# Optimization experiments

Measured on AMD Instinct MI355X. Metric: run time of the kernel, lower is better.

## Reference

```python
import jax, jax.numpy as jnp
import numpy as np

ALPHA = 0.3  # LeakyReLU negative slope
NEG_INF = -1e9


def setup_inputs() -> dict:
    key = jax.random.key(0)
    k1, k2, k3, k4 = jax.random.split(key, 4)
    B, N, C_IN, C_OUT, H = 4, 2048, 128, 128, 4
    node_feats = jax.random.normal(k1, (B, N, C_IN), dtype=jnp.float32)
    # xavier_uniform with gain 1.414 for projection weight [c_out, c_in]
    limit_w = 1.414 * np.sqrt(6.0 / (C_IN + C_OUT))
    W = jax.random.uniform(k2, (C_OUT, C_IN), minval=-limit_w, maxval=limit_w, dtype=jnp.float32)
    b = jnp.zeros((C_OUT,), dtype=jnp.float32)
    c_head = C_OUT // H
    limit_a = 1.414 * np.sqrt(6.0 / (H + 2 * c_head))
    a = jax.random.uniform(k3, (H, 2 * c_head), minval=-limit_a, maxval=limit_a, dtype=jnp.float32)
    return {"node_feats": node_feats, "W": W, "b": b, "a": a}


def reference(node_feats, W, b, a):
    B, N, _ = node_feats.shape
    H, two_c = a.shape
    c = two_c // 2
    # dynamic adjacency: cosine similarity, sigmoid > 0.5  <=>  sim > 0
    nf = node_feats / jnp.maximum(jnp.linalg.norm(node_feats, axis=-1, keepdims=True), 1e-12)
    sim = jnp.einsum('bid,bjd->bij', nf, nf)            # [B,N,N]
    mask = sim > 0.0                                     # adjacency (sigmoid(sim) > 0.5)
    # projection -> per-head features [B,N,H,c]
    h = (node_feats @ W.T + b).reshape(B, N, H, c)
    # edge score a . [h_i, h_j] decomposes into left/right parts
    a_l, a_r = a[:, :c], a[:, c:]                        # [H,c] each
    s_l = jnp.einsum('bnhc,hc->bnh', h, a_l)             # [B,N,H]
    s_r = jnp.einsum('bnhc,hc->bnh', h, a_r)             # [B,N,H]
    logits = jax.nn.leaky_relu(s_l[:, :, None, :] + s_r[:, None, :, :], ALPHA)  # [B,N,N,H]
    attn = jnp.where(mask[..., None], logits, NEG_INF)
    probs = jax.nn.softmax(attn, axis=2)                 # softmax over source nodes j
    # dropout is identity in eval mode
    out = jnp.einsum('bijh,bjhc->bihc', probs, h)
    return out.reshape(B, N, -1)                         # concat heads
```

## Files before the change

kernel.cpp:

```cpp
#include <hip/hip_runtime.h>
#include <cstdint>
#include <cstddef>

typedef float v16f __attribute__((ext_vector_type(16)));
typedef short v8s  __attribute__((ext_vector_type(8)));

#define MFMA32(A,B,C) __builtin_amdgcn_mfma_f32_32x32x16_bf16((A),(B),(C),0,0,0)
#define THRU 1e-3f

__device__ __forceinline__ unsigned f2bf(float f) {
  unsigned u = __builtin_bit_cast(unsigned, f);
  u += 0x7FFFu + ((u >> 16) & 1u);
  return u >> 16;
}
__device__ __forceinline__ float bf2f(unsigned us) {
  return __builtin_bit_cast(float, us << 16);
}
__device__ __forceinline__ void gload16(const void* g, void* l) {
  __builtin_amdgcn_global_load_lds(
      (const __attribute__((address_space(1))) void*)g,
      (__attribute__((address_space(3))) void*)l, 16, 0, 0);
}

__global__ __launch_bounds__(256) void gat_prep(
    const float* __restrict__ nf, const float* __restrict__ Wm,
    const float* __restrict__ bias, const float* __restrict__ aw,
    unsigned short* __restrict__ nfh, unsigned short* __restrict__ nfm,
    unsigned short* __restrict__ ht,
    float* __restrict__ EFl, float* __restrict__ EFh)
{
  __shared__ float xl[32][132];
  const int tid = threadIdx.x;
  const int row = tid & 31, g = tid >> 5;
  const int r0 = blockIdx.x * 32;
  const int b = r0 >> 11, n0 = r0 & 2047;
  const int d0 = g * 16;

  float x[16];
  {
    const float* xp = nf + (size_t)(r0 + row) * 128 + d0;
#pragma unroll
    for (int q = 0; q < 4; ++q) {
      float4 v = *(const float4*)(xp + 4 * q);
      x[4*q+0] = v.x; x[4*q+1] = v.y; x[4*q+2] = v.z; x[4*q+3] = v.w;
    }
  }
  {
    unsigned hu[16], mu[16];
#pragma unroll
    for (int q = 0; q < 16; ++q) {
      xl[row][d0 + q] = x[q];
      unsigned hb = f2bf(x[q]); float hf = bf2f(hb);
      unsigned mb = f2bf(x[q] - hf);
      hu[q] = hb; mu[q] = mb;
    }
    const size_t to = ((size_t)(b * 64 + (n0 >> 5)) * 8 + g) * 512 + row * 8;
    uint4 p0, p1;
    p0.x = hu[0] | (hu[1] << 16);  p0.y = hu[2] | (hu[3] << 16);
    p0.z = hu[4] | (hu[5] << 16);  p0.w = hu[6] | (hu[7] << 16);
    p1.x = hu[8] | (hu[9] << 16);  p1.y = hu[10] | (hu[11] << 16);
    p1.z = hu[12] | (hu[13] << 16); p1.w = hu[14] | (hu[15] << 16);
    *(uint4*)(nfh + to) = p0; *(uint4*)(nfh + to + 256) = p1;
    p0.x = mu[0] | (mu[1] << 16);  p0.y = mu[2] | (mu[3] << 16);
    p0.z = mu[4] | (mu[5] << 16);  p0.w = mu[6] | (mu[7] << 16);
    p1.x = mu[8] | (mu[9] << 16);  p1.y = mu[10] | (mu[11] << 16);
    p1.z = mu[12] | (mu[13] << 16); p1.w = mu[14] | (mu[15] << 16);
    *(uint4*)(nfm + to) = p0; *(uint4*)(nfm + to + 256) = p1;
  }
  __syncthreads();

  float acc[16];
  const int ob = g * 16;
#pragma unroll
  for (int o = 0; o < 16; ++o) acc[o] = bias[ob + o];
  for (int dd = 0; dd < 128; dd += 4) {
    float4 xq = *(const float4*)&xl[row][dd];
#pragma unroll
    for (int o = 0; o < 16; ++o) {
      float4 wq = *(const float4*)(Wm + (size_t)(ob + o) * 128 + dd);
      acc[o] = fmaf(xq.x, wq.x, acc[o]);
      acc[o] = fmaf(xq.y, wq.y, acc[o]);
      acc[o] = fmaf(xq.z, wq.z, acc[o]);
      acc[o] = fmaf(xq.w, wq.w, acc[o]);
    }
  }
#pragma unroll
  for (int o = 0; o < 16; ++o)
    ht[((size_t)b * 128 + ob + o) * 2048 + n0 + row] = (unsigned short)f2bf(acc[o]);

  const int hh = g >> 1, cb = (g & 1) * 16;
  float sl = 0.f, sr = 0.f;
#pragma unroll
  for (int o = 0; o < 16; ++o) {
    sl = fmaf(acc[o], aw[hh * 64 + cb + o], sl);
    sr = fmaf(acc[o], aw[hh * 64 + 32 + cb + o], sr);
  }
  sl += __shfl_xor(sl, 32, 64);
  sr += __shfl_xor(sr, 32, 64);
  if (!(g & 1)) {
    const float L2E = 1.4426950408889634f;
    float El = exp2f(sl * L2E), Fl = exp2f(sl * (0.3f * L2E));
    float Er = exp2f(sr * L2E), Fr = exp2f(sr * (0.3f * L2E));
    size_t nn = (size_t)(r0 + row);
    EFl[nn * 8 + hh]     = El;
    EFl[nn * 8 + 4 + hh] = Fl;
    const size_t eo = ((size_t)(b * 4 + hh) * 2048 + (n0 + row)) * 2;
    EFh[eo]     = Er;
    EFh[eo + 1] = Fr;
  }
}

__global__ __launch_bounds__(256) void gat_mask(
    const unsigned short* __restrict__ nfh, const unsigned short* __restrict__ nfm,
    const float* __restrict__ nf, unsigned* __restrict__ mask)
{
  const int tid = threadIdx.x, lane = tid & 63;
  const int li = lane & 31, hi = lane >> 5;
  const int blk = blockIdx.x;
  const int jb = blk & 31, t = blk >> 5;
  const int ib = t & 15, b = t >> 4;
  const int i0 = ib * 128 + (tid >> 6) * 32;
  const int j0 = jb * 64;

  const size_t lbyte = (size_t)lane * 8;
  const size_t tiB  = ((size_t)(b * 64 + (i0 >> 5)) * 8) * 512 + lbyte;
  const size_t tjA0 = ((size_t)(b * 64 + (j0 >> 5)) * 8) * 512 + lbyte;
  const size_t tjA1 = tjA0 + 4096;

  v8s BH[8], BM[8];
#pragma unroll
  for (int kc = 0; kc < 8; ++kc) {
    BH[kc] = *(const v8s*)(nfh + tiB + kc * 512);
    BM[kc] = *(const v8s*)(nfm + tiB + kc * 512);
  }

  v16f S0, S1;
#pragma unroll
  for (int r = 0; r < 16; ++r) { S0[r] = 0.f; S1[r] = 0.f; }
#pragma unroll
  for (int kc = 0; kc < 8; ++kc) {
    v8s A0h = *(const v8s*)(nfh + tjA0 + kc * 512);
    v8s A1h = *(const v8s*)(nfh + tjA1 + kc * 512);
    v8s A0m = *(const v8s*)(nfm + tjA0 + kc * 512);
    v8s A1m = *(const v8s*)(nfm + tjA1 + kc * 512);
    S0 = MFMA32(A0h, BH[kc], S0);
    S1 = MFMA32(A1h, BH[kc], S1);
    S0 = MFMA32(A0h, BM[kc], S0);
    S1 = MFMA32(A1h, BM[kc], S1);
    S0 = MFMA32(A0m, BH[kc], S0);
    S1 = MFMA32(A1m, BH[kc], S1);
  }

  unsigned u0 = 0, u1 = 0;
  float mn = 1e30f;
  const int sh = hi * 4;
#pragma unroll
  for (int r = 0; r < 16; ++r) {
    const int jlc = (r & 3) + 8 * (r >> 2);
    const unsigned bit = (1u << jlc) << sh;
    if (S0[r] > 0.f) u0 |= bit;
    if (S1[r] > 0.f) u1 |= bit;
    mn = fminf(mn, fabsf(S0[r]));
    mn = fminf(mn, fabsf(S1[r]));
  }

  if (mn < THRU) {
    const float* xi = nf + ((size_t)b * 2048 + i0 + li) * 128;
#pragma unroll
    for (int sub = 0; sub < 2; ++sub) {
#pragma unroll
      for (int r = 0; r < 16; ++r) {
        const float s = sub ? S1[r] : S0[r];
        if (fabsf(s) < THRU) {
          const int jlc = (r & 3) + 8 * (r >> 2);
          const int j = j0 + sub * 32 + jlc + 4 * hi;
          const float* xj = nf + ((size_t)b * 2048 + j) * 128;
          double a = 0.0;
          for (int k = 0; k < 128; k += 2) {
            a = fma((double)xi[k],     (double)xj[k],     a);
            a = fma((double)xi[k + 1], (double)xj[k + 1], a);
          }
          const unsigned bit = (1u << jlc) << sh;
          if (sub == 0) u0 = (a > 0.0) ? (u0 | bit) : (u0 & ~bit);
          else          u1 = (a > 0.0) ? (u1 | bit) : (u1 & ~bit);
        }
      }
    }
  }

  unsigned f0 = u0 | (unsigned)__shfl_xor((int)u0, 32, 64);
  unsigned f1 = u1 | (unsigned)__shfl_xor((int)u1, 32, 64);
  if (hi == 0) {
    mask[(size_t)(b * 64 + jb * 2)     * 2048 + i0 + li] = f0;
    mask[(size_t)(b * 64 + jb * 2 + 1) * 2048 + i0 + li] = f1;
  }
}

__global__ __launch_bounds__(256, 2) void gat_attn(
    const unsigned short* __restrict__ ht, const float* __restrict__ EFl,
    const float* __restrict__ EFh, const unsigned* __restrict__ mask,
    float* __restrict__ out)
{
  __shared__ __align__(16) char sm[36864];
  const int tid = threadIdx.x, lane = tid & 63, wv = tid >> 6;
  const int li = lane & 31, hi = lane >> 5;

  const int blk = blockIdx.x;
  const int ig = (blk >> 3) & 63;
  const int combo = (blk & 7) * 2 + (blk >> 9);
  const int b = combo >> 2, h = combo & 3;

  const size_t nb = (size_t)b * 2048;
  const int i0 = ig * 32;
  const int j0w = wv * 512;
  char* mybase = sm + wv * 9216;

  const float EL = EFl[(nb + i0 + li) * 8 + h];
  const float FL = EFl[(nb + i0 + li) * 8 + 4 + h];

  unsigned mw[16];
#pragma unroll
  for (int q = 0; q < 16; ++q)
    mw[q] = mask[(size_t)(b * 64 + wv * 16 + q) * 2048 + i0 + li] >> (hi * 4);

  asm volatile("s_waitcnt vmcnt(0)" ::: "memory");
  __builtin_amdgcn_sched_barrier(0);

  const int vrow = lane >> 3, vgs = lane & 7;
  auto STAGE = [&](int h0, int p) {
    const int jbase = j0w + (h0 << 6);
    const size_t srow = (size_t)(b * 128 + h * 32) * 2048 + jbase;
#pragma unroll
    for (int q = 0; q < 4; ++q) {
      const int row = q * 8 + vrow;
      gload16((const char*)(ht + srow + (size_t)row * 2048 + ((vgs ^ (row & 7)) << 3)),
              mybase + p * 4608 + q * 1024);
    }
    if (lane < 32)
      gload16((const char*)EFh + ((size_t)(b * 4 + h) * 2048 + jbase) * 8 + lane * 16,
              mybase + p * 4608 + 4096);
  };

  STAGE(0, 0);

  v16f acc;
#pragma unroll
  for (int r = 0; r < 16; ++r) acc[r] = 0.f;
  float den = 0.f;

#pragma unroll
  for (int h0 = 0; h0 < 8; ++h0) {
    const int p = h0 & 1;
    if (h0 < 7) {
      STAGE(h0 + 1, p ^ 1);
      asm volatile("s_waitcnt vmcnt(5)" ::: "memory");
    } else {
      asm volatile("s_waitcnt vmcnt(0)" ::: "memory");
    }
    __builtin_amdgcn_sched_barrier(0);

    const char* base = mybase + p * 4608;
#pragma unroll
    for (int it2 = 0; it2 < 2; ++it2) {
      const unsigned mh = mw[h0 * 2 + it2];
      const char* Eb = base + 4096 + (it2 << 8);
      unsigned pw[8];
#pragma unroll
      for (int rp = 0; rp < 8; ++rp) {
        const int r0 = 2 * rp;
        const int jl0c = (r0 & 3) + 8 * (r0 >> 2);
        const int off = (jl0c + 4 * hi) * 8;
        float2 e0 = *(const float2*)(Eb + off);
        float2 e1 = *(const float2*)(Eb + off + 8);
        const bool m0 = (mh >> jl0c) & 1;
        const bool m1 = (mh >> (jl0c + 1)) & 1;
        float w0 = fmaxf(e0.x * EL, e0.y * FL); w0 = m0 ? w0 : 0.f;
        float w1 = fmaxf(e1.x * EL, e1.y * FL); w1 = m1 ? w1 : 0.f;
        den += w0 + w1;
        asm("v_cvt_pk_bf16_f32 %0, %1, %2" : "=v"(pw[rp]) : "v"(w0), "v"(w1));
      }
      auto q0 = __builtin_amdgcn_permlane32_swap((int)pw[0], (int)pw[2], false, false);
      auto q1 = __builtin_amdgcn_permlane32_swap((int)pw[1], (int)pw[3], false, false);
      auto q2 = __builtin_amdgcn_permlane32_swap((int)pw[4], (int)pw[6], false, false);
      auto q3 = __builtin_amdgcn_permlane32_swap((int)pw[5], (int)pw[7], false, false);
      uint4 c0, c1;
      c0.x = (unsigned)q0[0]; c0.y = (unsigned)q1[0];
      c0.z = (unsigned)q0[1]; c0.w = (unsigned)q1[1];
      c1.x = (unsigned)q2[0]; c1.y = (unsigned)q3[0];
      c1.z = (unsigned)q2[1]; c1.w = (unsigned)q3[1];
      v8s P0 = __builtin_bit_cast(v8s, c0);
      v8s P1 = __builtin_bit_cast(v8s, c1);
      const char* vr = base + li * 128;
      const int cx = li & 7;
      v8s V0 = *(const v8s*)(vr + ((((it2 << 2) + hi) ^ cx) << 4));
      v8s V1 = *(const v8s*)(vr + ((((it2 << 2) + 2 + hi) ^ cx) << 4));
      acc = MFMA32(P0, V0, acc);
      acc = MFMA32(P1, V1, acc);
    }
  }

  __syncthreads();
  if (wv) {
    float* dst = (float*)sm + (size_t)(wv - 1) * 1088 + lane * 17;
#pragma unroll
    for (int r = 0; r < 16; ++r) dst[r] = acc[r];
    dst[16] = den;
  }
  __syncthreads();
  if (wv == 0) {
#pragma unroll
    for (int w = 0; w < 3; ++w) {
      const float* src = (const float*)sm + (size_t)w * 1088 + lane * 17;
#pragma unroll
      for (int r = 0; r < 16; ++r) acc[r] += src[r];
      den += src[16];
    }
    den += __shfl_xor(den, 32, 64);
    float* dl = (float*)sm + 3 * 1088;
    if (lane < 32) dl[li] = den;
    asm volatile("s_waitcnt lgkmcnt(0)" ::: "memory");
    __builtin_amdgcn_sched_barrier(0);
    const size_t ob = (nb + i0) * 128 + h * 32 + li;
#pragma unroll
    for (int r = 0; r < 16; ++r) {
      const int il = (r & 3) + 8 * (r >> 2) + 4 * hi;
      out[ob + (size_t)il * 128] = acc[r] / dl[il];
    }
  }
}

extern "C" void kernel_launch(void* const* d_in, const int* in_sizes, int n_in,
                              void* d_out, int out_size, void* d_ws, size_t ws_size,
                              hipStream_t stream) {
  const float* nf   = (const float*)d_in[0];
  const float* Wm   = (const float*)d_in[1];
  const float* bias = (const float*)d_in[2];
  const float* aw   = (const float*)d_in[3];
  float* out = (float*)d_out;
  char* ws = (char*)d_ws;

  unsigned short* nfh = (unsigned short*)(ws);
  unsigned short* nfm = (unsigned short*)(ws + 2097152);
  unsigned short* ht  = (unsigned short*)(ws + 4194304);
  float*    EFl  = (float*)(ws + 6291456);
  float*    EFh  = (float*)(ws + 6553600);
  unsigned* mask = (unsigned*)(ws + 6815744);

  gat_prep<<<256, 256, 0, stream>>>(nf, Wm, bias, aw, nfh, nfm, ht, EFl, EFh);
  gat_mask<<<2048, 256, 0, stream>>>(nfh, nfm, nf, mask);
  gat_attn<<<1024, 256, 0, stream>>>(ht, EFl, EFh, mask, out);
}
```

Before: 82.10 us.

## Store projected features in MFMA fragment layout and load directly from global

Result: slower. 88.74 us (+8.1%).

```diff
diff --git a/kernel.cpp b/kernel.cpp
--- a/kernel.cpp
+++ b/kernel.cpp
@@ -16,17 +16,12 @@
 __device__ __forceinline__ float bf2f(unsigned us) {
   return __builtin_bit_cast(float, us << 16);
 }
-__device__ __forceinline__ void gload16(const void* g, void* l) {
-  __builtin_amdgcn_global_load_lds(
-      (const __attribute__((address_space(1))) void*)g,
-      (__attribute__((address_space(3))) void*)l, 16, 0, 0);
-}
 
 __global__ __launch_bounds__(256) void gat_prep(
     const float* __restrict__ nf, const float* __restrict__ Wm,
     const float* __restrict__ bias, const float* __restrict__ aw,
     unsigned short* __restrict__ nfh, unsigned short* __restrict__ nfm,
-    unsigned short* __restrict__ ht,
+    unsigned short* __restrict__ vt,
     float* __restrict__ EFl, float* __restrict__ EFh)
 {
   __shared__ float xl[32][132];
@@ -84,9 +79,16 @@
       acc[o] = fmaf(xq.w, wq.w, acc[o]);
     }
   }
-#pragma unroll
-  for (int o = 0; o < 16; ++o)
-    ht[((size_t)b * 128 + ob + o) * 2048 + n0 + row] = (unsigned short)f2bf(acc[o]);
+  {
+    const int f = (row >> 4) & 1, kh = (row >> 3) & 1, e = row & 7;
+#pragma unroll
+    for (int o = 0; o < 16; ++o) {
+      const int c = ob + o, hh2 = c >> 5, cc = c & 31;
+      const size_t va = (((size_t)(b * 4 + hh2) * 64 + (n0 >> 5)) * 2 + f) * 512
+                        + (kh * 32 + cc) * 8 + e;
+      vt[va] = (unsigned short)f2bf(acc[o]);
+    }
+  }
 
   const int hh = g >> 1, cb = (g & 1) * 16;
   float sl = 0.f, sr = 0.f;
@@ -196,127 +198,100 @@
   }
 }
 
-__global__ __launch_bounds__(256, 2) void gat_attn(
-    const unsigned short* __restrict__ ht, const float* __restrict__ EFl,
+__global__ __launch_bounds__(256) void gat_attn(
+    const unsigned short* __restrict__ vt, const float* __restrict__ EFl,
     const float* __restrict__ EFh, const unsigned* __restrict__ mask,
     float* __restrict__ out)
 {
-  __shared__ __align__(16) char sm[36864];
+  __shared__ __align__(16) float sm[2][64][17];
   const int tid = threadIdx.x, lane = tid & 63, wv = tid >> 6;
   const int li = lane & 31, hi = lane >> 5;
 
   const int blk = blockIdx.x;
-  const int ig = (blk >> 3) & 63;
-  const int combo = (blk & 7) * 2 + (blk >> 9);
+  const int ig = blk & 63;
+  const int combo = blk >> 6;
   const int b = combo >> 2, h = combo & 3;
 
   const size_t nb = (size_t)b * 2048;
   const int i0 = ig * 32;
-  const int j0w = wv * 512;
-  char* mybase = sm + wv * 9216;
 
   const float EL = EFl[(nb + i0 + li) * 8 + h];
   const float FL = EFl[(nb + i0 + li) * 8 + 4 + h];
 
-  unsigned mw[16];
-#pragma unroll
-  for (int q = 0; q < 16; ++q)
-    mw[q] = mask[(size_t)(b * 64 + wv * 16 + q) * 2048 + i0 + li] >> (hi * 4);
-
-  asm volatile("s_waitcnt vmcnt(0)" ::: "memory");
-  __builtin_amdgcn_sched_barrier(0);
-
-  const int vrow = lane >> 3, vgs = lane & 7;
-  auto STAGE = [&](int h0, int p) {
-    const int jbase = j0w + (h0 << 6);
-    const size_t srow = (size_t)(b * 128 + h * 32) * 2048 + jbase;
-#pragma unroll
-    for (int q = 0; q < 4; ++q) {
-      const int row = q * 8 + vrow;
-      gload16((const char*)(ht + srow + (size_t)row * 2048 + ((vgs ^ (row & 7)) << 3)),
-              mybase + p * 4608 + q * 1024);
-    }
-    if (lane < 32)
-      gload16((const char*)EFh + ((size_t)(b * 4 + h) * 2048 + jbase) * 8 + lane * 16,
-              mybase + p * 4608 + 4096);
-  };
-
-  STAGE(0, 0);
+  const unsigned* mrow = mask + (size_t)(b * 64 + wv * 16) * 2048 + i0 + li;
+  const float* efb = EFh + ((size_t)(b * 4 + h) * 2048 + wv * 512) * 2;
+  const unsigned short* vb =
+      vt + ((size_t)(b * 4 + h) * 64 + wv * 16) * 1024 + (size_t)lane * 8;
 
   v16f acc;
 #pragma unroll
   for (int r = 0; r < 16; ++r) acc[r] = 0.f;
-  float den = 0.f;
-
-#pragma unroll
-  for (int h0 = 0; h0 < 8; ++h0) {
-    const int p = h0 & 1;
-    if (h0 < 7) {
-      STAGE(h0 + 1, p ^ 1);
-      asm volatile("s_waitcnt vmcnt(5)" ::: "memory");
-    } else {
-      asm volatile("s_waitcnt vmcnt(0)" ::: "memory");
-    }
-    __builtin_amdgcn_sched_barrier(0);
-
-    const char* base = mybase + p * 4608;
-#pragma unroll
-    for (int it2 = 0; it2 < 2; ++it2) {
-      const unsigned mh = mw[h0 * 2 + it2];
-      const char* Eb = base + 4096 + (it2 << 8);
-      unsigned pw[8];
-#pragma unroll
-      for (int rp = 0; rp < 8; ++rp) {
-        const int r0 = 2 * rp;
-        const int jl0c = (r0 & 3) + 8 * (r0 >> 2);
-        const int off = (jl0c + 4 * hi) * 8;
-        float2 e0 = *(const float2*)(Eb + off);
-        float2 e1 = *(const float2*)(Eb + off + 8);
-        const bool m0 = (mh >> jl0c) & 1;
-        const bool m1 = (mh >> (jl0c + 1)) & 1;
-        float w0 = fmaxf(e0.x * EL, e0.y * FL); w0 = m0 ? w0 : 0.f;
-        float w1 = fmaxf(e1.x * EL, e1.y * FL); w1 = m1 ? w1 : 0.f;
-        den += w0 + w1;
-        asm("v_cvt_pk_bf16_f32 %0, %1, %2" : "=v"(pw[rp]) : "v"(w0), "v"(w1));
-      }
-      auto q0 = __builtin_amdgcn_permlane32_swap((int)pw[0], (int)pw[2], false, false);
-      auto q1 = __builtin_amdgcn_permlane32_swap((int)pw[1], (int)pw[3], false, false);
-      auto q2 = __builtin_amdgcn_permlane32_swap((int)pw[4], (int)pw[6], false, false);
-      auto q3 = __builtin_amdgcn_permlane32_swap((int)pw[5], (int)pw[7], false, false);
-      uint4 c0, c1;
-      c0.x = (unsigned)q0[0]; c0.y = (unsigned)q1[0];
-      c0.z = (unsigned)q0[1]; c0.w = (unsigned)q1[1];
-      c1.x = (unsigned)q2[0]; c1.y = (unsigned)q3[0];
-      c1.z = (unsigned)q2[1]; c1.w = (unsigned)q3[1];
-      v8s P0 = __builtin_bit_cast(v8s, c0);
-      v8s P1 = __builtin_bit_cast(v8s, c1);
-      const char* vr = base + li * 128;
-      const int cx = li & 7;
-      v8s V0 = *(const v8s*)(vr + ((((it2 << 2) + hi) ^ cx) << 4));
-      v8s V1 = *(const v8s*)(vr + ((((it2 << 2) + 2 + hi) ^ cx) << 4));
-      acc = MFMA32(P0, V0, acc);
-      acc = MFMA32(P1, V1, acc);
-    }
-  }
-
-  __syncthreads();
-  if (wv) {
-    float* dst = (float*)sm + (size_t)(wv - 1) * 1088 + lane * 17;
-#pragma unroll
-    for (int r = 0; r < 16; ++r) dst[r] = acc[r];
-    dst[16] = den;
+  float den0 = 0.f, den1 = 0.f;
+
+#pragma unroll 4
+  for (int it2 = 0; it2 < 16; ++it2) {
+    const unsigned mh = mrow[(size_t)it2 * 2048] >> (hi * 4);
+    v8s V0 = *(const v8s*)(vb + it2 * 1024);
+    v8s V1 = *(const v8s*)(vb + it2 * 1024 + 512);
+    unsigned pw[8];
+#pragma unroll
+    for (int rp = 0; rp < 8; ++rp) {
+      const int r0 = 2 * rp;
+      const int jl0c = (r0 & 3) + 8 * (r0 >> 2);
+      const int j2 = it2 * 32 + jl0c + 4 * hi;
+      float4 e01 = *(const float4*)(efb + j2 * 2);
+      const bool m0 = (mh >> jl0c) & 1;
+      const bool m1 = (mh >> (jl0c + 1)) & 1;
+      float w0 = fmaxf(e01.x * EL, e01.y * FL); w0 = m0 ? w0 : 0.f;
+      float w1 = fmaxf(e01.z * EL, e01.w * FL); w1 = m1 ? w1 : 0.f;
+      den0 += w0; den1 += w1;
+      asm("v_cvt_pk_bf16_f32 %0, %1, %2" : "=v"(pw[rp]) : "v"(w0), "v"(w1));
+    }
+    auto q0 = __builtin_amdgcn_permlane32_swap((int)pw[0], (int)pw[2], false, false);
+    auto q1 = __builtin_amdgcn_permlane32_swap((int)pw[1], (int)pw[3], false, false);
+    auto q2 = __builtin_amdgcn_permlane32_swap((int)pw[4], (int)pw[6], false, false);
+    auto q3 = __builtin_amdgcn_permlane32_swap((int)pw[5], (int)pw[7], false, false);
+    uint4 c0, c1;
+    c0.x = (unsigned)q0[0]; c0.y = (unsigned)q1[0];
+    c0.z = (unsigned)q0[1]; c0.w = (unsigned)q1[1];
+    c1.x = (unsigned)q2[0]; c1.y = (unsigned)q3[0];
+    c1.z = (unsigned)q2[1]; c1.w = (unsigned)q3[1];
+    v8s P0 = __builtin_bit_cast(v8s, c0);
+    v8s P1 = __builtin_bit_cast(v8s, c1);
+    acc = MFMA32(P0, V0, acc);
+    acc = MFMA32(P1, V1, acc);
+  }
+  float den = den0 + den1;
+
+  __syncthreads();
+  if (wv >= 2) {
+    float* d = &sm[wv - 2][lane][0];
+#pragma unroll
+    for (int r = 0; r < 16; ++r) d[r] = acc[r];
+    d[16] = den;
+  }
+  __syncthreads();
+  if (wv < 2) {
+    const float* s = &sm[wv][lane][0];
+#pragma unroll
+    for (int r = 0; r < 16; ++r) acc[r] += s[r];
+    den += s[16];
+  }
+  __syncthreads();
+  if (wv == 1) {
+    float* d = &sm[0][lane][0];
+#pragma unroll
+    for (int r = 0; r < 16; ++r) d[r] = acc[r];
+    d[16] = den;
   }
   __syncthreads();
   if (wv == 0) {
-#pragma unroll
-    for (int w = 0; w < 3; ++w) {
-      const float* src = (const float*)sm + (size_t)w * 1088 + lane * 17;
-#pragma unroll
-      for (int r = 0; r < 16; ++r) acc[r] += src[r];
-      den += src[16];
-    }
+    const float* s = &sm[0][lane][0];
+#pragma unroll
+    for (int r = 0; r < 16; ++r) acc[r] += s[r];
+    den += s[16];
     den += __shfl_xor(den, 32, 64);
-    float* dl = (float*)sm + 3 * 1088;
+    float* dl = &sm[1][0][0];
     if (lane < 32) dl[li] = den;
     asm volatile("s_waitcnt lgkmcnt(0)" ::: "memory");
     __builtin_amdgcn_sched_barrier(0);
@@ -341,12 +316,12 @@
 
   unsigned short* nfh = (unsigned short*)(ws);
   unsigned short* nfm = (unsigned short*)(ws + 2097152);
-  unsigned short* ht  = (unsigned short*)(ws + 4194304);
+  unsigned short* vt  = (unsigned short*)(ws + 4194304);
   float*    EFl  = (float*)(ws + 6291456);
   float*    EFh  = (float*)(ws + 6553600);
   unsigned* mask = (unsigned*)(ws + 6815744);
 
-  gat_prep<<<256, 256, 0, stream>>>(nf, Wm, bias, aw, nfh, nfm, ht, EFl, EFh);
+  gat_prep<<<256, 256, 0, stream>>>(nf, Wm, bias, aw, nfh, nfm, vt, EFl, EFh);
   gat_mask<<<2048, 256, 0, stream>>>(nfh, nfm, nf, mask);
-  gat_attn<<<1024, 256, 0, stream>>>(ht, EFl, EFh, mask, out);
-}
+  gat_attn<<<1024, 256, 0, stream>>>(vt, EFl, EFh, mask, out);
+}
```
